# Optimization experiments

Hardware: AMD Instinct MI355X
Metric: run time of the kernel (lower is better)

Reference implementation:

```python
import jax, jax.numpy as jnp
import numpy as np


def conv1d_same(x, w, b):
    # x:[B,C,W], w:[O,I,K] -> [B,O,W] (stride 1, SAME padding, k=11,p=5)
    y = jax.lax.conv_general_dilated(x, w, (1,), 'SAME',
                                     dimension_numbers=('NCH', 'OIH', 'NCH'))
    return y + b[None, :, None]


def maxpool8(x):
    B, C, W = x.shape
    return x.reshape(B, C, W // 8, 8).max(axis=-1)


def encoder(x, p):
    back1 = jax.nn.relu(conv1d_same(x, p['e_c1_w'], p['e_c1_b']))   # [B,64,1280]
    h = maxpool8(back1)                                              # [B,64,160]
    back2 = jax.nn.relu(conv1d_same(h, p['e_c2_w'], p['e_c2_b']))   # [B,128,160]
    h = maxpool8(back2)                                              # [B,128,20]
    h = h.reshape(h.shape[0], -1)                                    # [B,2560]
    h = jax.nn.relu(h @ p['e_f1_w'].T + p['e_f1_b'])
    fea = jax.nn.sigmoid(h @ p['e_f2_w'].T + p['e_f2_b'])            # [B,64]
    return back1, back2, fea


def decoder(fea, back1, back2, p):
    h = jax.nn.relu(fea @ p['d_f1_w'].T + p['d_f1_b'])
    h = jax.nn.relu(h @ p['d_f2_w'].T + p['d_f2_b'])                 # [B,2560]
    h = h.reshape(h.shape[0], 128, 20)
    h = jnp.repeat(h, 8, axis=-1)                                    # nearest upsample -> 160
    h = jax.nn.relu(conv1d_same(jnp.concatenate([h, back2], 1), p['d_c2_w'], p['d_c2_b']))
    h = jnp.repeat(h, 8, axis=-1)                                    # -> 1280
    h = jax.nn.relu(conv1d_same(jnp.concatenate([h, back1], 1), p['d_c1_w'], p['d_c1_b']))
    return h                                                         # [B,2,1280]


def pairwise_kl(fea_s, fea_t, lab_s, lab_t, L):
    # Group rows by label. jnp.argsort is stable, so within each label the
    # original row order is preserved, exactly like torch boolean-mask gather.
    # Equal per-label counts are assumed (required by F.kl_div shape match).
    gs = fea_s[jnp.argsort(lab_s)].reshape(L, -1, fea_s.shape[-1])
    gt = fea_t[jnp.argsort(lab_t)].reshape(L, -1, fea_t.shape[-1])
    T = jnp.concatenate([gs, gt], axis=1)          # [L, M, D]
    logT = jnp.log(T)
    M = T.shape[1] * T.shape[2]
    # kl_div(t_i.log(), t_j) with reduction='mean' = mean(t_j*(log t_j - log t_i))
    A = jnp.sum(T * logT, axis=(1, 2)) / M         # [L]: mean(t_j log t_j)
    C = jnp.einsum('imd,jmd->ij', logT, T) / M     # C[i,j] = mean(t_j log t_i)
    kl = (L - 1) * A.sum() - (C.sum() - jnp.trace(C))  # sum over i != j
    return (kl / (L * L / 2.0))[None]              # shape [1] like torch.zeros(1)


def setup_inputs() -> dict:
    key = jax.random.key(0)
    ks = jax.random.split(key, 12)
    B, L, W = 256, 8, 1280

    def w(k, shape, fan_in):
        return (jax.random.normal(k, shape, jnp.float32) / np.sqrt(fan_in)).astype(jnp.float32)

    return {
        'x_source': jax.random.normal(ks[0], (B, 2, W), jnp.float32),
        'x_target': jax.random.normal(ks[1], (B, 2, W), jnp.float32),
        'x_s_label': jnp.arange(B, dtype=jnp.int32) % L,  # balanced labels
        'x_t_label': jnp.arange(B, dtype=jnp.int32) % L,
        'label_all': L,
        'e_c1_w': w(ks[2], (64, 2, 11), 2 * 11),    'e_c1_b': jnp.zeros(64, jnp.float32),
        'e_c2_w': w(ks[3], (128, 64, 11), 64 * 11), 'e_c2_b': jnp.zeros(128, jnp.float32),
        'e_f1_w': w(ks[4], (512, 2560), 2560),      'e_f1_b': jnp.zeros(512, jnp.float32),
        'e_f2_w': w(ks[5], (64, 512), 512),         'e_f2_b': jnp.zeros(64, jnp.float32),
        'd_f1_w': w(ks[6], (256, 64), 64),          'd_f1_b': jnp.zeros(256, jnp.float32),
        'd_f2_w': w(ks[7], (2560, 256), 256),       'd_f2_b': jnp.zeros(2560, jnp.float32),
        'd_c2_w': w(ks[8], (64, 256, 11), 256 * 11),'d_c2_b': jnp.zeros(64, jnp.float32),
        'd_c1_w': w(ks[9], (2, 128, 11), 128 * 11), 'd_c1_b': jnp.zeros(2, jnp.float32),
    }


def reference(x_source, x_target, x_s_label, x_t_label, label_all,
              e_c1_w, e_c1_b, e_c2_w, e_c2_b, e_f1_w, e_f1_b, e_f2_w, e_f2_b,
              d_f1_w, d_f1_b, d_f2_w, d_f2_b, d_c2_w, d_c2_b, d_c1_w, d_c1_b):
    p = {'e_c1_w': e_c1_w, 'e_c1_b': e_c1_b, 'e_c2_w': e_c2_w, 'e_c2_b': e_c2_b,
         'e_f1_w': e_f1_w, 'e_f1_b': e_f1_b, 'e_f2_w': e_f2_w, 'e_f2_b': e_f2_b,
         'd_f1_w': d_f1_w, 'd_f1_b': d_f1_b, 'd_f2_w': d_f2_w, 'd_f2_b': d_f2_b,
         'd_c2_w': d_c2_w, 'd_c2_b': d_c2_b, 'd_c1_w': d_c1_w, 'd_c1_b': d_c1_b}
    back1_s, back2_s, fea_s = encoder(x_source, p)
    back1_t, back2_t, fea_t = encoder(x_target, p)
    out_s = decoder(fea_s, back1_t, back2_t, p)
    out_t = decoder(fea_t, back1_s, back2_s, p)
    kl = pairwise_kl(fea_s, fea_t, x_s_label, x_t_label, label_all)
    return out_s, out_t, kl
```

## Files before the change

kernel.cpp:

```cpp
#include <hip/hip_runtime.h>
#include <hip/hip_bf16.h>
#include <math.h>

#define BB   256
#define W1c  1280
#define W2c  160
#define C1c  64
#define C2c  128
#define KKc  11
#define LLc  8
#define DDc  64
#define GSc  32

typedef __attribute__((ext_vector_type(8))) short short8;
typedef __attribute__((ext_vector_type(4))) float f32x4;
typedef unsigned short u16;

__device__ inline float b2f(u16 h) { return __uint_as_float(((unsigned)h) << 16); }
__device__ inline u16 f2b(float f) {
  unsigned u = __float_as_uint(f);
  return (u16)((u + 0x7fffu + ((u >> 16) & 1u)) >> 16);
}

#define PRE_W2P   90112
#define PRE_WD2P  270336
#define PRE_WD1P  292864
#define PRE_EF1   1603584
#define PRE_DF2   2258944
#define PRE_UPT   2521088
#define PRE_B2T   3569664
#define PRE_W1P   3571712
#define PRE_B1T   4096000
#define PRE_D2T   4161536
__global__ __launch_bounds__(256) void prep_k(const float* __restrict__ ec2w, const float* __restrict__ dc2w,
                       const float* __restrict__ dc1w, const float* __restrict__ ef1w,
                       const float* __restrict__ df2w, const float* __restrict__ ec1w,
                       u16* __restrict__ W2p, u16* __restrict__ Wd2p, u16* __restrict__ Wd1p,
                       u16* __restrict__ ef1wbf, u16* __restrict__ df2wbf, u16* __restrict__ W1p,
                       u16* __restrict__ upT_s, u16* __restrict__ upT_t,
                       u16* __restrict__ b2T_s, u16* __restrict__ b2T_t,
                       u16* __restrict__ b1T_s, u16* __restrict__ b1T_t,
                       u16* __restrict__ d2T_s, u16* __restrict__ d2T_t) {
  int idx = blockIdx.x * 256 + threadIdx.x;
  if (idx < PRE_W2P) {
    int k = idx / 8192, oc = (idx / 64) % 128, ic = idx % 64;
    W2p[idx] = f2b(ec2w[(oc * 64 + ic) * 11 + k]);
  } else if (idx < PRE_WD2P) {
    int j = idx - PRE_W2P;
    int k = j / 16384, oc = (j / 256) % 64, icc = j % 256;
    Wd2p[j] = f2b(dc2w[(oc * 256 + icc) * 11 + k]);
  } else if (idx < PRE_WD1P) {
    int j = idx - PRE_WD2P;
    int k = j / 2048, rem = j % 2048;
    int chunk = rem / 512, oc = (rem / 32) % 16, c = rem % 32;
    Wd1p[j] = (oc < 2) ? f2b(dc1w[((size_t)oc * 128 + chunk * 32 + c) * 11 + k]) : 0;
  } else if (idx < PRE_EF1) {
    int j = idx - PRE_WD1P;
    ef1wbf[j] = f2b(ef1w[j]);
  } else if (idx < PRE_DF2) {
    int j = idx - PRE_EF1;
    df2wbf[j] = f2b(df2w[j]);
  } else if (idx < PRE_UPT) {
    int j = idx - PRE_DF2;
    int ic = j % 128, r4 = (j / 128) % 4, b = (j / 512) % 256, side = j / 131072;
    int row = (r4 == 0) ? 0 : (20 + r4);
    (side ? upT_t : upT_s)[((size_t)b * 24 + row) * 128 + ic] = 0;
  } else if (idx < PRE_B2T) {
    int j = idx - PRE_UPT;
    int ic = j % 128, pr = (j / 128) % 16, b = (j / 2048) % 256, side = j / 524288;
    int row = (pr < 8) ? pr : pr + 160;
    (side ? b2T_t : b2T_s)[((size_t)b * 176 + row) * 128 + ic] = 0;
  } else if (idx < PRE_W1P) {
    int j = idx - PRE_B2T;
    int oc = j >> 5, kk = j & 31, ic = kk >> 4, k = kk & 15;
    W1p[j] = (k < 11) ? f2b(ec1w[oc * 22 + ic * 11 + k]) : 0;
  } else if (idx < PRE_B1T) {
    int j = idx - PRE_W1P;
    int ic = j % 64, pr = (j / 64) % 16, b = (j / 1024) % 256, side = j / 262144;
    int row = (pr < 5) ? pr : 1280 + pr;
    (side ? b1T_t : b1T_s)[((size_t)b * 1296 + row) * 64 + ic] = 0;
  } else if (idx < PRE_D2T) {
    int j = idx - PRE_B1T;
    int ic = j % 64, pr = (j / 64) & 1, b = (j / 128) % 256, side = j / 32768;
    int row = pr ? 161 : 0;
    (side ? d2T_t : d2T_s)[((size_t)b * 162 + row) * 64 + ic] = 0;
  }
}

__global__ __launch_bounds__(256) void im2col1_k(const float* __restrict__ x, u16* __restrict__ xcol) {
  int idx = blockIdx.x * 256 + threadIdx.x;
  int wg = idx % 160, ic = (idx / 160) & 1, b = idx / 320;
  int w0 = wg * 8;
  const float* xb = x + (size_t)(b * 2 + ic) * 1280;
  u16 win[18];
#pragma unroll
  for (int j = 0; j < 18; j++) {
    int p = w0 - 5 + j;
    win[j] = (p >= 0 && p < 1280) ? f2b(xb[p]) : 0;
  }
#pragma unroll
  for (int r = 0; r < 8; r++) {
    uint4 s0, s1;
    s0.x = (unsigned)win[r + 0] | ((unsigned)win[r + 1] << 16);
    s0.y = (unsigned)win[r + 2] | ((unsigned)win[r + 3] << 16);
    s0.z = (unsigned)win[r + 4] | ((unsigned)win[r + 5] << 16);
    s0.w = (unsigned)win[r + 6] | ((unsigned)win[r + 7] << 16);
    s1.x = (unsigned)win[r + 8] | ((unsigned)win[r + 9] << 16);
    s1.y = (unsigned)win[r + 10];
    s1.z = 0; s1.w = 0;
    u16* dst = xcol + ((size_t)(b * 1280 + w0 + r) * 32 + ic * 16);
    *(uint4*)dst = s0;
    *(uint4*)(dst + 8) = s1;
  }
}

__global__ __launch_bounds__(256) void conv1_mfma(const u16* __restrict__ xcol, const u16* __restrict__ W1p,
                           const float* __restrict__ bias, u16* __restrict__ back1T) {
  int blk = blockIdx.x;
  int b = blk >> 2, wq = blk & 3;
  int tid = threadIdx.x, wid = tid >> 6, l = tid & 63;
  int l15 = l & 15, lq = l >> 4;
  int oc0 = wid * 16;
  int w0 = wq * 320;
  short8 a = *(const short8*)(W1p + (oc0 + l15) * 32 + lq * 8);
  f32x4 zero = {0.f, 0.f, 0.f, 0.f};
  f32x4 acc[20];
#pragma unroll
  for (int j = 0; j < 20; j++) acc[j] = zero;
  const u16* xb = xcol + (size_t)b * 1280 * 32;
#pragma unroll
  for (int nf = 0; nf < 20; nf++) {
    int w = w0 + nf * 16 + l15;
    short8 bf = *(const short8*)(xb + (size_t)w * 32 + lq * 8);
    acc[nf] = __builtin_amdgcn_mfma_f32_16x16x32_bf16(a, bf, acc[nf], 0, 0, 0);
  }
  int ocb = oc0 + lq * 4;
  float b0 = bias[ocb], b1 = bias[ocb + 1], b2 = bias[ocb + 2], b3 = bias[ocb + 3];
#pragma unroll
  for (int nf = 0; nf < 20; nf++) {
    int w = w0 + nf * 16 + l15;
    uint2 st;
    st.x = (unsigned)f2b(fmaxf(acc[nf][0] + b0, 0.f)) | ((unsigned)f2b(fmaxf(acc[nf][1] + b1, 0.f)) << 16);
    st.y = (unsigned)f2b(fmaxf(acc[nf][2] + b2, 0.f)) | ((unsigned)f2b(fmaxf(acc[nf][3] + b3, 0.f)) << 16);
    *(uint2*)(back1T + ((size_t)b * 1296 + w + 5) * 64 + ocb) = st;
  }
}

__global__ __launch_bounds__(256) void pool1T_k(const u16* __restrict__ back1T, u16* __restrict__ p1T) {
  int idx = blockIdx.x * 256 + threadIdx.x;
  int ic = idx % 64, row = (idx / 64) % 176, b = idx / 11264;
  u16 val = 0;
  if (row >= 8 && row < 168) {
    const u16* pp = back1T + ((size_t)b * 1296 + (row - 8) * 8 + 5) * 64 + ic;
    float m = b2f(pp[0]);
#pragma unroll
    for (int j = 1; j < 8; j++) m = fmaxf(m, b2f(pp[j * 64]));
    val = f2b(m);
  }
  p1T[idx] = val;
}

__global__ __launch_bounds__(256) void conv2_mfma(const u16* __restrict__ p1T, const u16* __restrict__ W2p,
                           const float* __restrict__ bias, u16* __restrict__ back2T) {
  __shared__ u16 smem[90 * 72];
  int blk = blockIdx.x;
  int b = blk >> 1, wh = blk & 1;
  int tid = threadIdx.x, wid = tid >> 6, l = tid & 63;
  int l15 = l & 15, lq = l >> 4;
  int oc0 = wid * 32;
  int w0 = wh * 80;
  const u16* pb = p1T + (size_t)b * 176 * 64;
  for (int i = tid; i < 720; i += 256) {
    int row = i >> 3, seg = i & 7;
    *(uint4*)(&smem[row * 72 + seg * 8]) = *(const uint4*)(pb + ((size_t)(w0 + 3 + row)) * 64 + seg * 8);
  }
  __syncthreads();
  f32x4 zero = {0.f, 0.f, 0.f, 0.f};
  f32x4 acc[2][5];
#pragma unroll
  for (int i = 0; i < 2; i++)
#pragma unroll
    for (int j = 0; j < 5; j++) acc[i][j] = zero;
  for (int k = 0; k < 11; k++) {
    for (int ic0 = 0; ic0 < 64; ic0 += 32) {
      short8 a0 = *(const short8*)(W2p + ((k * 128 + oc0 + l15) * 64 + ic0 + lq * 8));
      short8 a1 = *(const short8*)(W2p + ((k * 128 + oc0 + 16 + l15) * 64 + ic0 + lq * 8));
      short8 bf[5];
#pragma unroll
      for (int nf = 0; nf < 5; nf++)
        bf[nf] = *(const short8*)(&smem[(nf * 16 + l15 + k) * 72 + ic0 + lq * 8]);
#pragma unroll
      for (int nf = 0; nf < 5; nf++) {
        acc[0][nf] = __builtin_amdgcn_mfma_f32_16x16x32_bf16(a0, bf[nf], acc[0][nf], 0, 0, 0);
        acc[1][nf] = __builtin_amdgcn_mfma_f32_16x16x32_bf16(a1, bf[nf], acc[1][nf], 0, 0, 0);
      }
    }
  }
#pragma unroll
  for (int mf = 0; mf < 2; mf++) {
    int ocb = oc0 + mf * 16 + lq * 4;
    float b0 = bias[ocb], b1 = bias[ocb + 1], b2 = bias[ocb + 2], b3 = bias[ocb + 3];
#pragma unroll
    for (int nf = 0; nf < 5; nf++) {
      int w = w0 + nf * 16 + l15;
      f32x4 v = acc[mf][nf];
      unsigned r0 = (unsigned)f2b(fmaxf(v[0] + b0, 0.f)) | ((unsigned)f2b(fmaxf(v[1] + b1, 0.f)) << 16);
      unsigned r1 = (unsigned)f2b(fmaxf(v[2] + b2, 0.f)) | ((unsigned)f2b(fmaxf(v[3] + b3, 0.f)) << 16);
      uint2 st; st.x = r0; st.y = r1;
      *(uint2*)(back2T + ((size_t)(b * 176 + 8 + w) * 128 + ocb)) = st;
    }
  }
}

__global__ __launch_bounds__(256) void pool2_k(const u16* __restrict__ b2T, u16* __restrict__ pool2bf) {
  int idx = blockIdx.x * 256 + threadIdx.x;
  int wo = idx % 20, oc = (idx / 20) % 128, b = idx / 2560;
  float m = -1e30f;
#pragma unroll
  for (int j = 0; j < 8; j++)
    m = fmaxf(m, b2f(b2T[((size_t)b * 176 + 8 + wo * 8 + j) * 128 + oc]));
  pool2bf[idx] = f2b(m);
}

__global__ __launch_bounds__(256) void ef1_split(const u16* __restrict__ A_s, const u16* __restrict__ A_t,
                          const u16* __restrict__ Bw, float* __restrict__ pbuf) {
  int blk = blockIdx.x;
  int side = blk >> 8;
  int r = blk & 255;
  int kc = r >> 5;
  int q = r & 31;
  int n0 = (q & 7) * 64;
  int tid = threadIdx.x, wid = tid >> 6, l = tid & 63;
  int l15 = l & 15, lq = l >> 4;
  int m0 = (q >> 3) * 64 + wid * 16;
  const u16* A = side ? A_t : A_s;
  f32x4 zero = {0.f, 0.f, 0.f, 0.f};
  f32x4 acc[4];
#pragma unroll
  for (int j = 0; j < 4; j++) acc[j] = zero;
  int kbase = kc * 320;
  for (int k0 = kbase; k0 < kbase + 320; k0 += 32) {
    short8 af = *(const short8*)(A + ((size_t)(m0 + l15) * 2560 + k0 + lq * 8));
    short8 bf[4];
#pragma unroll
    for (int nf = 0; nf < 4; nf++)
      bf[nf] = *(const short8*)(Bw + ((size_t)(n0 + nf * 16 + l15) * 2560 + k0 + lq * 8));
#pragma unroll
    for (int nf = 0; nf < 4; nf++)
      acc[nf] = __builtin_amdgcn_mfma_f32_16x16x32_bf16(af, bf[nf], acc[nf], 0, 0, 0);
  }
  int bb = m0 + lq * 4;
  float* pb = pbuf + (size_t)(side * 8 + kc) * 131072;
#pragma unroll
  for (int nf = 0; nf < 4; nf++) {
    int oc = n0 + nf * 16 + l15;
#pragma unroll
    for (int rr = 0; rr < 4; rr++)
      pb[(size_t)(bb + rr) * 512 + oc] = acc[nf][rr];
  }
}

__global__ __launch_bounds__(256) void ef1_red(const float* __restrict__ pbuf, const float* __restrict__ bias,
                        float* __restrict__ ef1_s, float* __restrict__ ef1_t) {
  int e = blockIdx.x * 256 + threadIdx.x;
  int side = e >> 17;
  int j = e & 131071;
  const float* pb = pbuf + (size_t)side * 8 * 131072;
  float s = 0.f;
#pragma unroll
  for (int kc = 0; kc < 8; kc++) s += pb[(size_t)kc * 131072 + j];
  s += bias[j & 511];
  (side ? ef1_t : ef1_s)[j] = fmaxf(s, 0.f);
}

__global__ __launch_bounds__(256) void ef2df1_k(const float* __restrict__ ef1, const float* __restrict__ ef2w,
                         const float* __restrict__ ef2b, const float* __restrict__ df1w,
                         const float* __restrict__ df1b, float* __restrict__ fea,
                         u16* __restrict__ df1bf) {
  __shared__ float row[512];
  __shared__ float part[256];
  __shared__ float fea_sh[64];
  int b = blockIdx.x, tid = threadIdx.x;
  row[tid] = ef1[(size_t)b * 512 + tid];
  row[tid + 256] = ef1[(size_t)b * 512 + tid + 256];
  __syncthreads();
  {
    int o = tid & 63, q = tid >> 6;
    const float4* wr = (const float4*)(ef2w + (size_t)o * 512 + q * 128);
    float s = 0.f;
    int base = q * 128;
#pragma unroll
    for (int i = 0; i < 32; i++) {
      float4 wv = wr[i];
      s += row[base + 4 * i] * wv.x + row[base + 4 * i + 1] * wv.y +
           row[base + 4 * i + 2] * wv.z + row[base + 4 * i + 3] * wv.w;
    }
    part[q * 64 + o] = s;
  }
  __syncthreads();
  if (tid < 64) {
    float v = part[tid] + part[64 + tid] + part[128 + tid] + part[192 + tid] + ef2b[tid];
    float sg = 1.f / (1.f + expf(-v));
    fea_sh[tid] = sg;
    fea[(size_t)b * 64 + tid] = sg;
  }
  __syncthreads();
  {
    const float4* wr = (const float4*)(df1w + (size_t)tid * 64);
    float s = 0.f;
#pragma unroll
    for (int i = 0; i < 16; i++) {
      float4 wv = wr[i];
      s += fea_sh[4 * i] * wv.x + fea_sh[4 * i + 1] * wv.y +
           fea_sh[4 * i + 2] * wv.z + fea_sh[4 * i + 3] * wv.w;
    }
    df1bf[(size_t)b * 256 + tid] = f2b(fmaxf(s + df1b[tid], 0.f));
  }
}

__global__ __launch_bounds__(256) void df2_gemm(const u16* __restrict__ A, const u16* __restrict__ Bw,
                         const float* __restrict__ bias, u16* __restrict__ upT) {
  int n0 = blockIdx.x * 64;
  int tid = threadIdx.x, wid = tid >> 6, l = tid & 63;
  int l15 = l & 15, lq = l >> 4;
  int m0 = wid * 64;
  f32x4 zero = {0.f, 0.f, 0.f, 0.f};
  f32x4 acc[4][4];
#pragma unroll
  for (int i = 0; i < 4; i++)
#pragma unroll
    for (int j = 0; j < 4; j++) acc[i][j] = zero;
  for (int k0 = 0; k0 < 256; k0 += 32) {
    short8 af[4], bf[4];
#pragma unroll
    for (int mf = 0; mf < 4; mf++)
      af[mf] = *(const short8*)(A + ((size_t)(m0 + mf * 16 + l15) * 256 + k0 + lq * 8));
#pragma unroll
    for (int nf = 0; nf < 4; nf++)
      bf[nf] = *(const short8*)(Bw + ((size_t)(n0 + nf * 16 + l15) * 256 + k0 + lq * 8));
#pragma unroll
    for (int mf = 0; mf < 4; mf++)
#pragma unroll
      for (int nf = 0; nf < 4; nf++)
        acc[mf][nf] = __builtin_amdgcn_mfma_f32_16x16x32_bf16(af[mf], bf[nf], acc[mf][nf], 0, 0, 0);
  }
#pragma unroll
  for (int nf = 0; nf < 4; nf++) {
    int o = n0 + nf * 16 + l15;
    float bi = bias[o];
    int ch = o / 20, t = o - ch * 20;
#pragma unroll
    for (int mf = 0; mf < 4; mf++) {
      int bb = m0 + mf * 16 + lq * 4;
#pragma unroll
      for (int r = 0; r < 4; r++)
        upT[((size_t)(bb + r) * 24 + 1 + t) * 128 + ch] = f2b(fmaxf(acc[mf][nf][r] + bi, 0.f));
    }
  }
}

__global__ __launch_bounds__(256) void convd2_mfma(const u16* __restrict__ upT, const u16* __restrict__ skipT,
                            const u16* __restrict__ Wd2p, const float* __restrict__ bias,
                            u16* __restrict__ dc2T) {
  __shared__ u16 smem[90 * 136];
  int blk = blockIdx.x;
  int b = blk >> 1, wh = blk & 1;
  int tid = threadIdx.x, wid = tid >> 6, l = tid & 63;
  int l15 = l & 15, lq = l >> 4;
  int oc0 = wid * 16;
  int w0 = wh * 80;
  const u16* sb = skipT + (size_t)b * 176 * 128;
  for (int i = tid; i < 1440; i += 256) {
    int row = i >> 4, seg = i & 15;
    *(uint4*)(&smem[row * 136 + seg * 8]) = *(const uint4*)(sb + ((size_t)(w0 + 3 + row)) * 128 + seg * 8);
  }
  __syncthreads();
  f32x4 zero = {0.f, 0.f, 0.f, 0.f};
  f32x4 acc[5];
#pragma unroll
  for (int j = 0; j < 5; j++) acc[j] = zero;
  const u16* ub = upT + (size_t)b * 24 * 128;
  for (int k = 0; k < 11; k++) {
    for (int ic0 = 0; ic0 < 128; ic0 += 32) {
      short8 a = *(const short8*)(Wd2p + ((k * 64 + oc0 + l15) * 256 + ic0 + lq * 8));
#pragma unroll
      for (int nf = 0; nf < 5; nf++) {
        int w = w0 + nf * 16 + l15;
        int r = (w + k + 3) >> 3;
        short8 bf = *(const short8*)(ub + (r * 128 + ic0 + lq * 8));
        acc[nf] = __builtin_amdgcn_mfma_f32_16x16x32_bf16(a, bf, acc[nf], 0, 0, 0);
      }
    }
    for (int ic0 = 0; ic0 < 128; ic0 += 32) {
      short8 a = *(const short8*)(Wd2p + ((k * 64 + oc0 + l15) * 256 + 128 + ic0 + lq * 8));
#pragma unroll
      for (int nf = 0; nf < 5; nf++) {
        short8 bf = *(const short8*)(&smem[(nf * 16 + l15 + k) * 136 + ic0 + lq * 8]);
        acc[nf] = __builtin_amdgcn_mfma_f32_16x16x32_bf16(a, bf, acc[nf], 0, 0, 0);
      }
    }
  }
  int ocb = oc0 + lq * 4;
  float bb0 = bias[ocb], bb1 = bias[ocb + 1], bb2 = bias[ocb + 2], bb3 = bias[ocb + 3];
#pragma unroll
  for (int nf = 0; nf < 5; nf++) {
    int w = w0 + nf * 16 + l15;
    uint2 st;
    st.x = (unsigned)f2b(fmaxf(acc[nf][0] + bb0, 0.f)) | ((unsigned)f2b(fmaxf(acc[nf][1] + bb1, 0.f)) << 16);
    st.y = (unsigned)f2b(fmaxf(acc[nf][2] + bb2, 0.f)) | ((unsigned)f2b(fmaxf(acc[nf][3] + bb3, 0.f)) << 16);
    *(uint2*)(dc2T + ((size_t)b * 162 + w + 1) * 64 + ocb) = st;
  }
}

__global__ __launch_bounds__(256) void convd1_mfma(const u16* __restrict__ dc2T, const u16* __restrict__ back1T,
                            const u16* __restrict__ Wd1p, const float* __restrict__ bias,
                            float* __restrict__ out) {
  __shared__ u16 smem[330 * 72];
  int blk = blockIdx.x;
  int b = blk >> 2, q = blk & 3;
  int tid = threadIdx.x, wid = tid >> 6, l = tid & 63;
  int l15 = l & 15, lq = l >> 4;
  int base = q * 320;
  int wloc0 = wid * 80;
  const u16* sb = back1T + (size_t)b * 1296 * 64;
  for (int i = tid; i < 2640; i += 256) {
    int row = i >> 3, seg = i & 7;
    *(uint4*)(&smem[row * 72 + seg * 8]) = *(const uint4*)(sb + ((size_t)(base + row)) * 64 + seg * 8);
  }
  __syncthreads();
  f32x4 zero = {0.f, 0.f, 0.f, 0.f};
  f32x4 acc[5];
#pragma unroll
  for (int j = 0; j < 5; j++) acc[j] = zero;
  const u16* ub = dc2T + (size_t)b * 162 * 64;
  for (int k = 0; k < 11; k++) {
#pragma unroll
    for (int ch = 0; ch < 2; ch++) {
      short8 wf = *(const short8*)(Wd1p + ((k * 4 + ch) * 16 + l15) * 32 + lq * 8);
#pragma unroll
      for (int nf = 0; nf < 5; nf++) {
        int w = base + wloc0 + nf * 16 + l15;
        int r = (w + k + 3) >> 3;
        short8 af = *(const short8*)(ub + (r * 64 + ch * 32 + lq * 8));
        acc[nf] = __builtin_amdgcn_mfma_f32_16x16x32_bf16(af, wf, acc[nf], 0, 0, 0);
      }
    }
#pragma unroll
    for (int ch = 0; ch < 2; ch++) {
      short8 wf = *(const short8*)(Wd1p + ((k * 4 + 2 + ch) * 16 + l15) * 32 + lq * 8);
#pragma unroll
      for (int nf = 0; nf < 5; nf++) {
        int lrow = wloc0 + nf * 16 + l15 + k;
        short8 af = *(const short8*)(&smem[lrow * 72 + ch * 32 + lq * 8]);
        acc[nf] = __builtin_amdgcn_mfma_f32_16x16x32_bf16(af, wf, acc[nf], 0, 0, 0);
      }
    }
  }
  if (l15 < 2) {
    float bi = bias[l15];
    float* ob = out + ((size_t)b * 2 + l15) * 1280;
#pragma unroll
    for (int nf = 0; nf < 5; nf++) {
      int wbase = base + wloc0 + nf * 16 + lq * 4;
      float4 v;
      v.x = fmaxf(acc[nf][0] + bi, 0.f);
      v.y = fmaxf(acc[nf][1] + bi, 0.f);
      v.z = fmaxf(acc[nf][2] + bi, 0.f);
      v.w = fmaxf(acc[nf][3] + bi, 0.f);
      *(float4*)(ob + wbase) = v;
    }
  }
}

__global__ void kl_sort_k(const int* __restrict__ lab_s, const int* __restrict__ lab_t,
                          int* __restrict__ srt) {
  int t = threadIdx.x;
  {
    int lab = lab_s[t];
    int pos = 0;
    for (int b = 0; b < BB; b++) {
      int lb = lab_s[b];
      pos += (lb < lab) + ((b < t) && (lb == lab));
    }
    srt[pos] = t;
  }
  {
    int lab = lab_t[t];
    int pos = 0;
    for (int b = 0; b < BB; b++) {
      int lb = lab_t[b];
      pos += (lb < lab) + ((b < t) && (lb == lab));
    }
    srt[256 + pos] = t;
  }
}

__global__ void kl_build_k(const float* __restrict__ fea_s, const float* __restrict__ fea_t,
                           const int* __restrict__ srt,
                           float* __restrict__ T, float* __restrict__ logT) {
  int idx = blockIdx.x * 256 + threadIdx.x;
#pragma unroll
  for (int r = 0; r < 4; r++) {
    int e = idx + r * 8192;
    int d = e & 63;
    int m = (e >> 6) & 63;
    int l = e >> 12;
    float v;
    if (m < GSc) v = fea_s[srt[l * GSc + m] * DDc + d];
    else         v = fea_t[srt[256 + l * GSc + (m - GSc)] * DDc + d];
    T[e]    = v;
    logT[e] = logf(v);
  }
}

__global__ void kl_pairs_k(const float* __restrict__ T, const float* __restrict__ logT,
                           float* __restrict__ C) {
  int blk = blockIdx.x;
  int i = blk >> 3, j = blk & 7;
  int t = threadIdx.x;
  __shared__ float wsum[4];
  const float* li = logT + i * 4096;
  const float* tj = T + j * 4096;
  float s = 0.f;
  for (int e = t; e < 4096; e += 256) s += li[e] * tj[e];
  for (int off = 32; off > 0; off >>= 1) s += __shfl_down(s, off, 64);
  if ((t & 63) == 0) wsum[t >> 6] = s;
  __syncthreads();
  if (t == 0) C[blk] = wsum[0] + wsum[1] + wsum[2] + wsum[3];
}

__global__ void kl_final_k(const float* __restrict__ C, float* __restrict__ out) {
  int t = threadIdx.x;
  float c = C[t];
  float tr = ((t >> 3) == (t & 7)) ? c : 0.f;
  for (int off = 32; off > 0; off >>= 1) {
    c  += __shfl_down(c, off, 64);
    tr += __shfl_down(tr, off, 64);
  }
  if (t == 0) out[0] = (LLc * tr - c) / 4096.f / (LLc * LLc / 2.0f);
}

extern "C" void kernel_launch(void* const* d_in, const int* in_sizes, int n_in,
                              void* d_out, int out_size, void* d_ws, size_t ws_size,
                              hipStream_t stream) {
  const float* x_s  = (const float*)d_in[0];
  const float* x_t  = (const float*)d_in[1];
  const int* lab_s  = (const int*)d_in[2];
  const int* lab_t  = (const int*)d_in[3];
  const float* ec1w = (const float*)d_in[5];  const float* ec1b = (const float*)d_in[6];
  const float* ec2w = (const float*)d_in[7];  const float* ec2b = (const float*)d_in[8];
  const float* ef1w = (const float*)d_in[9];  const float* ef1b = (const float*)d_in[10];
  const float* ef2w = (const float*)d_in[11]; const float* ef2b = (const float*)d_in[12];
  const float* df1w = (const float*)d_in[13]; const float* df1b = (const float*)d_in[14];
  const float* df2w = (const float*)d_in[15]; const float* df2b = (const float*)d_in[16];
  const float* dc2w = (const float*)d_in[17]; const float* dc2b = (const float*)d_in[18];
  const float* dc1w = (const float*)d_in[19]; const float* dc1b = (const float*)d_in[20];

  char* p = (char*)d_ws;
  auto alloc = [&](size_t bytes) -> char* {
    char* r = p;
    p += (bytes + 255) & ~(size_t)255;
    return r;
  };
  u16*   b1T_s   = (u16*)alloc((size_t)BB * 1296 * 64 * 2);
  u16*   b1T_t   = (u16*)alloc((size_t)BB * 1296 * 64 * 2);
  u16*   xcol_s  = (u16*)alloc((size_t)BB * 1280 * 32 * 2);
  u16*   xcol_t  = (u16*)alloc((size_t)BB * 1280 * 32 * 2);
  u16*   p1T_s   = (u16*)alloc((size_t)BB * 176 * 64 * 2);
  u16*   p1T_t   = (u16*)alloc((size_t)BB * 176 * 64 * 2);
  u16*   b2T_s   = (u16*)alloc((size_t)BB * 176 * 128 * 2);
  u16*   b2T_t   = (u16*)alloc((size_t)BB * 176 * 128 * 2);
  u16*   upT_s   = (u16*)alloc((size_t)BB * 24 * 128 * 2);
  u16*   upT_t   = (u16*)alloc((size_t)BB * 24 * 128 * 2);
  u16*   p2bf_s  = (u16*)alloc((size_t)BB * 2560 * 2);
  u16*   p2bf_t  = (u16*)alloc((size_t)BB * 2560 * 2);
  float* ef1_s   = (float*)alloc((size_t)BB * 512 * 4);
  float* ef1_t   = (float*)alloc((size_t)BB * 512 * 4);
  float* fea_s   = (float*)alloc((size_t)BB * 64 * 4);
  float* fea_t   = (float*)alloc((size_t)BB * 64 * 4);
  u16*   df1bf_s = (u16*)alloc((size_t)BB * 256 * 2);
  u16*   df1bf_t = (u16*)alloc((size_t)BB * 256 * 2);
  u16*   d2T_s   = (u16*)alloc((size_t)BB * 162 * 64 * 2);
  u16*   d2T_t   = (u16*)alloc((size_t)BB * 162 * 64 * 2);
  u16*   W2p     = (u16*)alloc(90112 * 2);
  u16*   Wd2p    = (u16*)alloc(180224 * 2);
  u16*   Wd1p    = (u16*)alloc(22528 * 2);
  u16*   ef1wbf  = (u16*)alloc((size_t)1310720 * 2);
  u16*   df2wbf  = (u16*)alloc((size_t)655360 * 2);
  u16*   W1p     = (u16*)alloc(2048 * 2);
  float* Tbuf    = (float*)alloc((size_t)32768 * 4);
  float* logTbuf = (float*)alloc((size_t)32768 * 4);
  int*   srt     = (int*)alloc(512 * 4);
  float* Cbuf    = (float*)alloc(64 * 4);
  float* pbuf    = (float*)xcol_s;

  float* out_s  = (float*)d_out;
  float* out_t  = out_s + (size_t)BB * 2 * 1280;
  float* out_kl = out_s + (size_t)2 * BB * 2 * 1280;

  dim3 blk(256);

  prep_k<<<dim3(16256), blk, 0, stream>>>(ec2w, dc2w, dc1w, ef1w, df2w, ec1w,
                                          W2p, Wd2p, Wd1p, ef1wbf, df2wbf, W1p,
                                          upT_s, upT_t, b2T_s, b2T_t,
                                          b1T_s, b1T_t, d2T_s, d2T_t);

  im2col1_k<<<dim3(320), blk, 0, stream>>>(x_s, xcol_s);
  im2col1_k<<<dim3(320), blk, 0, stream>>>(x_t, xcol_t);
  conv1_mfma<<<dim3(1024), blk, 0, stream>>>(xcol_s, W1p, ec1b, b1T_s);
  conv1_mfma<<<dim3(1024), blk, 0, stream>>>(xcol_t, W1p, ec1b, b1T_t);
  pool1T_k<<<dim3(11264), blk, 0, stream>>>(b1T_s, p1T_s);
  pool1T_k<<<dim3(11264), blk, 0, stream>>>(b1T_t, p1T_t);
  conv2_mfma<<<dim3(512), blk, 0, stream>>>(p1T_s, W2p, ec2b, b2T_s);
  conv2_mfma<<<dim3(512), blk, 0, stream>>>(p1T_t, W2p, ec2b, b2T_t);
  pool2_k<<<dim3(2560), blk, 0, stream>>>(b2T_s, p2bf_s);
  pool2_k<<<dim3(2560), blk, 0, stream>>>(b2T_t, p2bf_t);

  ef1_split<<<dim3(512), blk, 0, stream>>>(p2bf_s, p2bf_t, ef1wbf, pbuf);
  ef1_red<<<dim3(1024), blk, 0, stream>>>(pbuf, ef1b, ef1_s, ef1_t);

  ef2df1_k<<<dim3(256), blk, 0, stream>>>(ef1_s, ef2w, ef2b, df1w, df1b, fea_s, df1bf_s);
  ef2df1_k<<<dim3(256), blk, 0, stream>>>(ef1_t, ef2w, ef2b, df1w, df1b, fea_t, df1bf_t);

  df2_gemm<<<dim3(40), blk, 0, stream>>>(df1bf_s, df2wbf, df2b, upT_s);
  df2_gemm<<<dim3(40), blk, 0, stream>>>(df1bf_t, df2wbf, df2b, upT_t);

  convd2_mfma<<<dim3(512), blk, 0, stream>>>(upT_s, b2T_t, Wd2p, dc2b, d2T_s);
  convd2_mfma<<<dim3(512), blk, 0, stream>>>(upT_t, b2T_s, Wd2p, dc2b, d2T_t);

  convd1_mfma<<<dim3(1024), blk, 0, stream>>>(d2T_s, b1T_t, Wd1p, dc1b, out_s);
  convd1_mfma<<<dim3(1024), blk, 0, stream>>>(d2T_t, b1T_s, Wd1p, dc1b, out_t);

  kl_sort_k<<<dim3(1), blk, 0, stream>>>(lab_s, lab_t, srt);
  kl_build_k<<<dim3(32), blk, 0, stream>>>(fea_s, fea_t, srt, Tbuf, logTbuf);
  kl_pairs_k<<<dim3(64), blk, 0, stream>>>(Tbuf, logTbuf, Cbuf);
  kl_final_k<<<dim3(1), dim3(64), 0, stream>>>(Cbuf, out_kl);
}
```

Baseline: 525.9 us.

## Merge source/target kernel launches and split conv2/convd2 work across more blocks

Each pair of per-side launches is merged into one grid that picks the source or target buffers from the block index, which halves the launch count and fills more of the GPU per launch. conv2 is split by output-channel half so each block has 4x more blocks in the grid with fewer accumulators. convd2 is split over halves of the kernel taps into fp32 partial sums stored in the reused xcol_t buffer, followed by a new reduction kernel that applies bias and relu. The partial-sum round trip adds memory traffic and an extra launch in exchange for more parallelism.

After: 489.7 us. -6.9%, faster.

```diff
diff --git a/kernel.cpp b/kernel.cpp
--- a/kernel.cpp
+++ b/kernel.cpp
@@ -3,11 +3,6 @@
 #include <math.h>
 
 #define BB   256
-#define W1c  1280
-#define W2c  160
-#define C1c  64
-#define C2c  128
-#define KKc  11
 #define LLc  8
 #define DDc  64
 #define GSc  32
@@ -87,11 +82,15 @@
   }
 }
 
-__global__ __launch_bounds__(256) void im2col1_k(const float* __restrict__ x, u16* __restrict__ xcol) {
-  int idx = blockIdx.x * 256 + threadIdx.x;
+__global__ __launch_bounds__(256) void im2col1_k(const float* __restrict__ x_s, const float* __restrict__ x_t,
+                          u16* __restrict__ xcol_s, u16* __restrict__ xcol_t) {
+  int bk = blockIdx.x;
+  int side = bk >= 320;
+  int idx = (bk - (side ? 320 : 0)) * 256 + threadIdx.x;
   int wg = idx % 160, ic = (idx / 160) & 1, b = idx / 320;
   int w0 = wg * 8;
-  const float* xb = x + (size_t)(b * 2 + ic) * 1280;
+  const float* xb = (side ? x_t : x_s) + (size_t)(b * 2 + ic) * 1280;
+  u16* xcol = side ? xcol_t : xcol_s;
   u16 win[18];
 #pragma unroll
   for (int j = 0; j < 18; j++) {
@@ -114,10 +113,15 @@
   }
 }
 
-__global__ __launch_bounds__(256) void conv1_mfma(const u16* __restrict__ xcol, const u16* __restrict__ W1p,
-                           const float* __restrict__ bias, u16* __restrict__ back1T) {
+__global__ __launch_bounds__(256) void conv1_mfma(const u16* __restrict__ xcol_s, const u16* __restrict__ xcol_t,
+                           const u16* __restrict__ W1p, const float* __restrict__ bias,
+                           u16* __restrict__ b1T_s, u16* __restrict__ b1T_t) {
   int blk = blockIdx.x;
-  int b = blk >> 2, wq = blk & 3;
+  int side = blk >> 10;
+  int r = blk & 1023;
+  int b = r >> 2, wq = r & 3;
+  const u16* xcol = side ? xcol_t : xcol_s;
+  u16* back1T = side ? b1T_t : b1T_s;
   int tid = threadIdx.x, wid = tid >> 6, l = tid & 63;
   int l15 = l & 15, lq = l >> 4;
   int oc0 = wid * 16;
@@ -146,9 +150,13 @@
   }
 }
 
-__global__ __launch_bounds__(256) void pool1T_k(const u16* __restrict__ back1T, u16* __restrict__ p1T) {
-  int idx = blockIdx.x * 256 + threadIdx.x;
+__global__ __launch_bounds__(256) void pool1T_k(const u16* __restrict__ b1T_s, const u16* __restrict__ b1T_t,
+                         u16* __restrict__ p1T_s, u16* __restrict__ p1T_t) {
+  int bk = blockIdx.x;
+  int side = bk >= 11264;
+  int idx = (bk - (side ? 11264 : 0)) * 256 + threadIdx.x;
   int ic = idx % 64, row = (idx / 64) % 176, b = idx / 11264;
+  const u16* back1T = side ? b1T_t : b1T_s;
   u16 val = 0;
   if (row >= 8 && row < 168) {
     const u16* pp = back1T + ((size_t)b * 1296 + (row - 8) * 8 + 5) * 64 + ic;
@@ -157,17 +165,22 @@
     for (int j = 1; j < 8; j++) m = fmaxf(m, b2f(pp[j * 64]));
     val = f2b(m);
   }
-  p1T[idx] = val;
-}
-
-__global__ __launch_bounds__(256) void conv2_mfma(const u16* __restrict__ p1T, const u16* __restrict__ W2p,
-                           const float* __restrict__ bias, u16* __restrict__ back2T) {
+  (side ? p1T_t : p1T_s)[idx] = val;
+}
+
+__global__ __launch_bounds__(256) void conv2_split(const u16* __restrict__ p1T_s, const u16* __restrict__ p1T_t,
+                            const u16* __restrict__ W2p, const float* __restrict__ bias,
+                            u16* __restrict__ b2T_s, u16* __restrict__ b2T_t) {
   __shared__ u16 smem[90 * 72];
   int blk = blockIdx.x;
-  int b = blk >> 1, wh = blk & 1;
+  int side = blk >> 10;
+  int r = blk & 1023;
+  int b = r >> 2, wh = (r >> 1) & 1, oh = r & 1;
+  const u16* p1T = side ? p1T_t : p1T_s;
+  u16* back2T = side ? b2T_t : b2T_s;
   int tid = threadIdx.x, wid = tid >> 6, l = tid & 63;
   int l15 = l & 15, lq = l >> 4;
-  int oc0 = wid * 32;
+  int oc0 = oh * 64 + wid * 16;
   int w0 = wh * 80;
   const u16* pb = p1T + (size_t)b * 176 * 64;
   for (int i = tid; i < 720; i += 256) {
@@ -176,50 +189,46 @@
   }
   __syncthreads();
   f32x4 zero = {0.f, 0.f, 0.f, 0.f};
-  f32x4 acc[2][5];
-#pragma unroll
-  for (int i = 0; i < 2; i++)
-#pragma unroll
-    for (int j = 0; j < 5; j++) acc[i][j] = zero;
+  f32x4 acc[5];
+#pragma unroll
+  for (int j = 0; j < 5; j++) acc[j] = zero;
   for (int k = 0; k < 11; k++) {
     for (int ic0 = 0; ic0 < 64; ic0 += 32) {
-      short8 a0 = *(const short8*)(W2p + ((k * 128 + oc0 + l15) * 64 + ic0 + lq * 8));
-      short8 a1 = *(const short8*)(W2p + ((k * 128 + oc0 + 16 + l15) * 64 + ic0 + lq * 8));
+      short8 a = *(const short8*)(W2p + ((k * 128 + oc0 + l15) * 64 + ic0 + lq * 8));
       short8 bf[5];
 #pragma unroll
       for (int nf = 0; nf < 5; nf++)
         bf[nf] = *(const short8*)(&smem[(nf * 16 + l15 + k) * 72 + ic0 + lq * 8]);
 #pragma unroll
-      for (int nf = 0; nf < 5; nf++) {
-        acc[0][nf] = __builtin_amdgcn_mfma_f32_16x16x32_bf16(a0, bf[nf], acc[0][nf], 0, 0, 0);
-        acc[1][nf] = __builtin_amdgcn_mfma_f32_16x16x32_bf16(a1, bf[nf], acc[1][nf], 0, 0, 0);
-      }
-    }
-  }
-#pragma unroll
-  for (int mf = 0; mf < 2; mf++) {
-    int ocb = oc0 + mf * 16 + lq * 4;
-    float b0 = bias[ocb], b1 = bias[ocb + 1], b2 = bias[ocb + 2], b3 = bias[ocb + 3];
-#pragma unroll
-    for (int nf = 0; nf < 5; nf++) {
-      int w = w0 + nf * 16 + l15;
-      f32x4 v = acc[mf][nf];
-      unsigned r0 = (unsigned)f2b(fmaxf(v[0] + b0, 0.f)) | ((unsigned)f2b(fmaxf(v[1] + b1, 0.f)) << 16);
-      unsigned r1 = (unsigned)f2b(fmaxf(v[2] + b2, 0.f)) | ((unsigned)f2b(fmaxf(v[3] + b3, 0.f)) << 16);
-      uint2 st; st.x = r0; st.y = r1;
-      *(uint2*)(back2T + ((size_t)(b * 176 + 8 + w) * 128 + ocb)) = st;
-    }
-  }
-}
-
-__global__ __launch_bounds__(256) void pool2_k(const u16* __restrict__ b2T, u16* __restrict__ pool2bf) {
-  int idx = blockIdx.x * 256 + threadIdx.x;
+      for (int nf = 0; nf < 5; nf++)
+        acc[nf] = __builtin_amdgcn_mfma_f32_16x16x32_bf16(a, bf[nf], acc[nf], 0, 0, 0);
+    }
+  }
+  int ocb = oc0 + lq * 4;
+  float b0 = bias[ocb], b1 = bias[ocb + 1], b2 = bias[ocb + 2], b3 = bias[ocb + 3];
+#pragma unroll
+  for (int nf = 0; nf < 5; nf++) {
+    int w = w0 + nf * 16 + l15;
+    f32x4 v = acc[nf];
+    uint2 st;
+    st.x = (unsigned)f2b(fmaxf(v[0] + b0, 0.f)) | ((unsigned)f2b(fmaxf(v[1] + b1, 0.f)) << 16);
+    st.y = (unsigned)f2b(fmaxf(v[2] + b2, 0.f)) | ((unsigned)f2b(fmaxf(v[3] + b3, 0.f)) << 16);
+    *(uint2*)(back2T + ((size_t)(b * 176 + 8 + w) * 128 + ocb)) = st;
+  }
+}
+
+__global__ __launch_bounds__(256) void pool2_k(const u16* __restrict__ b2T_s, const u16* __restrict__ b2T_t,
+                        u16* __restrict__ p2bf_s, u16* __restrict__ p2bf_t) {
+  int bk = blockIdx.x;
+  int side = bk >= 2560;
+  int idx = (bk - (side ? 2560 : 0)) * 256 + threadIdx.x;
   int wo = idx % 20, oc = (idx / 20) % 128, b = idx / 2560;
+  const u16* b2T = side ? b2T_t : b2T_s;
   float m = -1e30f;
 #pragma unroll
   for (int j = 0; j < 8; j++)
     m = fmaxf(m, b2f(b2T[((size_t)b * 176 + 8 + wo * 8 + j) * 128 + oc]));
-  pool2bf[idx] = f2b(m);
+  (side ? p2bf_t : p2bf_s)[idx] = f2b(m);
 }
 
 __global__ __launch_bounds__(256) void ef1_split(const u16* __restrict__ A_s, const u16* __restrict__ A_t,
@@ -273,14 +282,20 @@
   (side ? ef1_t : ef1_s)[j] = fmaxf(s, 0.f);
 }
 
-__global__ __launch_bounds__(256) void ef2df1_k(const float* __restrict__ ef1, const float* __restrict__ ef2w,
-                         const float* __restrict__ ef2b, const float* __restrict__ df1w,
-                         const float* __restrict__ df1b, float* __restrict__ fea,
-                         u16* __restrict__ df1bf) {
+__global__ __launch_bounds__(256) void ef2df1_k(const float* __restrict__ ef1_s, const float* __restrict__ ef1_t,
+                         const float* __restrict__ ef2w, const float* __restrict__ ef2b,
+                         const float* __restrict__ df1w, const float* __restrict__ df1b,
+                         float* __restrict__ fea_s, float* __restrict__ fea_t,
+                         u16* __restrict__ df1bf_s, u16* __restrict__ df1bf_t) {
   __shared__ float row[512];
   __shared__ float part[256];
   __shared__ float fea_sh[64];
-  int b = blockIdx.x, tid = threadIdx.x;
+  int side = blockIdx.x >> 8;
+  int b = blockIdx.x & 255;
+  const float* ef1 = side ? ef1_t : ef1_s;
+  float* fea = side ? fea_t : fea_s;
+  u16* df1bf = side ? df1bf_t : df1bf_s;
+  int tid = threadIdx.x;
   row[tid] = ef1[(size_t)b * 512 + tid];
   row[tid + 256] = ef1[(size_t)b * 512 + tid + 256];
   __syncthreads();
@@ -318,9 +333,14 @@
   }
 }
 
-__global__ __launch_bounds__(256) void df2_gemm(const u16* __restrict__ A, const u16* __restrict__ Bw,
-                         const float* __restrict__ bias, u16* __restrict__ upT) {
-  int n0 = blockIdx.x * 64;
+__global__ __launch_bounds__(256) void df2_gemm(const u16* __restrict__ A_s, const u16* __restrict__ A_t,
+                         const u16* __restrict__ Bw, const float* __restrict__ bias,
+                         u16* __restrict__ upT_s, u16* __restrict__ upT_t) {
+  int blk = blockIdx.x;
+  int side = blk >= 40;
+  int n0 = (blk - (side ? 40 : 0)) * 64;
+  const u16* A = side ? A_t : A_s;
+  u16* upT = side ? upT_t : upT_s;
   int tid = threadIdx.x, wid = tid >> 6, l = tid & 63;
   int l15 = l & 15, lq = l >> 4;
   int m0 = wid * 64;
@@ -359,12 +379,16 @@
   }
 }
 
-__global__ __launch_bounds__(256) void convd2_mfma(const u16* __restrict__ upT, const u16* __restrict__ skipT,
-                            const u16* __restrict__ Wd2p, const float* __restrict__ bias,
-                            u16* __restrict__ dc2T) {
+__global__ __launch_bounds__(256) void convd2_split(const u16* __restrict__ upT_s, const u16* __restrict__ upT_t,
+                             const u16* __restrict__ b2T_s, const u16* __restrict__ b2T_t,
+                             const u16* __restrict__ Wd2p, float* __restrict__ part) {
   __shared__ u16 smem[90 * 136];
   int blk = blockIdx.x;
-  int b = blk >> 1, wh = blk & 1;
+  int side = blk >> 10;
+  int r = blk & 1023;
+  int b = r >> 2, wh = (r >> 1) & 1, khalf = r & 1;
+  const u16* upT   = side ? upT_t : upT_s;
+  const u16* skipT = side ? b2T_s : b2T_t;
   int tid = threadIdx.x, wid = tid >> 6, l = tid & 63;
   int l15 = l & 15, lq = l >> 4;
   int oc0 = wid * 16;
@@ -380,14 +404,15 @@
 #pragma unroll
   for (int j = 0; j < 5; j++) acc[j] = zero;
   const u16* ub = upT + (size_t)b * 24 * 128;
-  for (int k = 0; k < 11; k++) {
+  int kbeg = khalf ? 6 : 0, kend = khalf ? 11 : 6;
+  for (int k = kbeg; k < kend; k++) {
     for (int ic0 = 0; ic0 < 128; ic0 += 32) {
       short8 a = *(const short8*)(Wd2p + ((k * 64 + oc0 + l15) * 256 + ic0 + lq * 8));
 #pragma unroll
       for (int nf = 0; nf < 5; nf++) {
         int w = w0 + nf * 16 + l15;
-        int r = (w + k + 3) >> 3;
-        short8 bf = *(const short8*)(ub + (r * 128 + ic0 + lq * 8));
+        int rr = (w + k + 3) >> 3;
+        short8 bf = *(const short8*)(ub + (rr * 128 + ic0 + lq * 8));
         acc[nf] = __builtin_amdgcn_mfma_f32_16x16x32_bf16(a, bf, acc[nf], 0, 0, 0);
       }
     }
@@ -400,24 +425,47 @@
       }
     }
   }
+  float* pp = part + (((size_t)(side * 2 + khalf) * 256 + b) * 160) * 64;
   int ocb = oc0 + lq * 4;
-  float bb0 = bias[ocb], bb1 = bias[ocb + 1], bb2 = bias[ocb + 2], bb3 = bias[ocb + 3];
 #pragma unroll
   for (int nf = 0; nf < 5; nf++) {
     int w = w0 + nf * 16 + l15;
-    uint2 st;
-    st.x = (unsigned)f2b(fmaxf(acc[nf][0] + bb0, 0.f)) | ((unsigned)f2b(fmaxf(acc[nf][1] + bb1, 0.f)) << 16);
-    st.y = (unsigned)f2b(fmaxf(acc[nf][2] + bb2, 0.f)) | ((unsigned)f2b(fmaxf(acc[nf][3] + bb3, 0.f)) << 16);
-    *(uint2*)(dc2T + ((size_t)b * 162 + w + 1) * 64 + ocb) = st;
-  }
-}
-
-__global__ __launch_bounds__(256) void convd1_mfma(const u16* __restrict__ dc2T, const u16* __restrict__ back1T,
+    *(f32x4*)(pp + (size_t)w * 64 + ocb) = acc[nf];
+  }
+}
+
+__global__ __launch_bounds__(256) void convd2_red(const float* __restrict__ part, const float* __restrict__ bias,
+                           u16* __restrict__ d2T_s, u16* __restrict__ d2T_t) {
+  int idx = blockIdx.x * 256 + threadIdx.x;
+  int oc4 = (idx & 15) * 4;
+  int w = (idx >> 4) % 160;
+  int rb = (idx >> 4) / 160;
+  int b = rb & 255;
+  int side = rb >> 8;
+  const float* p0 = part + (((size_t)(side * 2 + 0) * 256 + b) * 160 + w) * 64 + oc4;
+  const float* p1 = part + (((size_t)(side * 2 + 1) * 256 + b) * 160 + w) * 64 + oc4;
+  float4 a = *(const float4*)p0;
+  float4 c = *(const float4*)p1;
+  float b0 = bias[oc4], b1 = bias[oc4 + 1], b2 = bias[oc4 + 2], b3 = bias[oc4 + 3];
+  uint2 st;
+  st.x = (unsigned)f2b(fmaxf(a.x + c.x + b0, 0.f)) | ((unsigned)f2b(fmaxf(a.y + c.y + b1, 0.f)) << 16);
+  st.y = (unsigned)f2b(fmaxf(a.z + c.z + b2, 0.f)) | ((unsigned)f2b(fmaxf(a.w + c.w + b3, 0.f)) << 16);
+  u16* dst = side ? d2T_t : d2T_s;
+  *(uint2*)(dst + ((size_t)b * 162 + w + 1) * 64 + oc4) = st;
+}
+
+__global__ __launch_bounds__(256) void convd1_mfma(const u16* __restrict__ d2T_s, const u16* __restrict__ d2T_t,
+                            const u16* __restrict__ b1T_s, const u16* __restrict__ b1T_t,
                             const u16* __restrict__ Wd1p, const float* __restrict__ bias,
-                            float* __restrict__ out) {
+                            float* __restrict__ out_s, float* __restrict__ out_t) {
   __shared__ u16 smem[330 * 72];
   int blk = blockIdx.x;
-  int b = blk >> 2, q = blk & 3;
+  int side = blk >> 10;
+  int r = blk & 1023;
+  int b = r >> 2, q = r & 3;
+  const u16* dc2T   = side ? d2T_t : d2T_s;
+  const u16* back1T = side ? b1T_s : b1T_t;
+  float* out = side ? out_t : out_s;
   int tid = threadIdx.x, wid = tid >> 6, l = tid & 63;
   int l15 = l & 15, lq = l >> 4;
   int base = q * 320;
@@ -440,8 +488,8 @@
 #pragma unroll
       for (int nf = 0; nf < 5; nf++) {
         int w = base + wloc0 + nf * 16 + l15;
-        int r = (w + k + 3) >> 3;
-        short8 af = *(const short8*)(ub + (r * 64 + ch * 32 + lq * 8));
+        int rr = (w + k + 3) >> 3;
+        short8 af = *(const short8*)(ub + (rr * 64 + ch * 32 + lq * 8));
         acc[nf] = __builtin_amdgcn_mfma_f32_16x16x32_bf16(af, wf, acc[nf], 0, 0, 0);
       }
     }
@@ -593,6 +641,7 @@
   int*   srt     = (int*)alloc(512 * 4);
   float* Cbuf    = (float*)alloc(64 * 4);
   float* pbuf    = (float*)xcol_s;
+  float* part    = (float*)xcol_t;
 
   float* out_s  = (float*)d_out;
   float* out_t  = out_s + (size_t)BB * 2 * 1280;
@@ -605,31 +654,20 @@
                                           upT_s, upT_t, b2T_s, b2T_t,
                                           b1T_s, b1T_t, d2T_s, d2T_t);
 
-  im2col1_k<<<dim3(320), blk, 0, stream>>>(x_s, xcol_s);
-  im2col1_k<<<dim3(320), blk, 0, stream>>>(x_t, xcol_t);
-  conv1_mfma<<<dim3(1024), blk, 0, stream>>>(xcol_s, W1p, ec1b, b1T_s);
-  conv1_mfma<<<dim3(1024), blk, 0, stream>>>(xcol_t, W1p, ec1b, b1T_t);
-  pool1T_k<<<dim3(11264), blk, 0, stream>>>(b1T_s, p1T_s);
-  pool1T_k<<<dim3(11264), blk, 0, stream>>>(b1T_t, p1T_t);
-  conv2_mfma<<<dim3(512), blk, 0, stream>>>(p1T_s, W2p, ec2b, b2T_s);
-  conv2_mfma<<<dim3(512), blk, 0, stream>>>(p1T_t, W2p, ec2b, b2T_t);
-  pool2_k<<<dim3(2560), blk, 0, stream>>>(b2T_s, p2bf_s);
-  pool2_k<<<dim3(2560), blk, 0, stream>>>(b2T_t, p2bf_t);
-
+  im2col1_k<<<dim3(640), blk, 0, stream>>>(x_s, x_t, xcol_s, xcol_t);
+  conv1_mfma<<<dim3(2048), blk, 0, stream>>>(xcol_s, xcol_t, W1p, ec1b, b1T_s, b1T_t);
+  pool1T_k<<<dim3(22528), blk, 0, stream>>>(b1T_s, b1T_t, p1T_s, p1T_t);
+  conv2_split<<<dim3(2048), blk, 0, stream>>>(p1T_s, p1T_t, W2p, ec2b, b2T_s, b2T_t);
+  pool2_k<<<dim3(5120), blk, 0, stream>>>(b2T_s, b2T_t, p2bf_s, p2bf_t);
   ef1_split<<<dim3(512), blk, 0, stream>>>(p2bf_s, p2bf_t, ef1wbf, pbuf);
   ef1_red<<<dim3(1024), blk, 0, stream>>>(pbuf, ef1b, ef1_s, ef1_t);
-
-  ef2df1_k<<<dim3(256), blk, 0, stream>>>(ef1_s, ef2w, ef2b, df1w, df1b, fea_s, df1bf_s);
-  ef2df1_k<<<dim3(256), blk, 0, stream>>>(ef1_t, ef2w, ef2b, df1w, df1b, fea_t, df1bf_t);
-
-  df2_gemm<<<dim3(40), blk, 0, stream>>>(df1bf_s, df2wbf, df2b, upT_s);
-  df2_gemm<<<dim3(40), blk, 0, stream>>>(df1bf_t, df2wbf, df2b, upT_t);
-
-  convd2_mfma<<<dim3(512), blk, 0, stream>>>(upT_s, b2T_t, Wd2p, dc2b, d2T_s);
-  convd2_mfma<<<dim3(512), blk, 0, stream>>>(upT_t, b2T_s, Wd2p, dc2b, d2T_t);
-
-  convd1_mfma<<<dim3(1024), blk, 0, stream>>>(d2T_s, b1T_t, Wd1p, dc1b, out_s);
-  convd1_mfma<<<dim3(1024), blk, 0, stream>>>(d2T_t, b1T_s, Wd1p, dc1b, out_t);
+  ef2df1_k<<<dim3(512), blk, 0, stream>>>(ef1_s, ef1_t, ef2w, ef2b, df1w, df1b,
+                                          fea_s, fea_t, df1bf_s, df1bf_t);
+
+  df2_gemm<<<dim3(80), blk, 0, stream>>>(df1bf_s, df1bf_t, df2wbf, df2b, upT_s, upT_t);
+  convd2_split<<<dim3(2048), blk, 0, stream>>>(upT_s, upT_t, b2T_s, b2T_t, Wd2p, part);
+  convd2_red<<<dim3(5120), blk, 0, stream>>>(part, dc2b, d2T_s, d2T_t);
+  convd1_mfma<<<dim3(2048), blk, 0, stream>>>(d2T_s, d2T_t, b1T_s, b1T_t, Wd1p, dc1b, out_s, out_t);
 
   kl_sort_k<<<dim3(1), blk, 0, stream>>>(lab_s, lab_t, srt);
   kl_build_k<<<dim3(32), blk, 0, stream>>>(fea_s, fea_t, srt, Tbuf, logTbuf);
```
